# Kernel tuning notes

Measured on AMD Instinct MI355X. Metric: run time of the kernel, lower is better.

Reference implementation:

```python
import jax, jax.numpy as jnp
import numpy as np

NUM_CLASSES = 21
THRESHOLD = 0.5
VAR0, VAR1 = 0.1, 0.2
NEGPOS_RATIO = 3


def setup_inputs() -> dict:
    key = jax.random.key(0)
    k1, k2, k3, k4, k5, k6, k7 = jax.random.split(key, 7)
    B, P, C, O = 64, 8732, 21, 8
    loc_data = jax.random.normal(k1, (B, P, 4), dtype=jnp.float32) * 0.1
    conf_data = jax.random.normal(k2, (B, P, C), dtype=jnp.float32)
    # priors: center form (cx, cy, w, h), valid in [0,1]
    cxy = jax.random.uniform(k3, (P, 2), minval=0.05, maxval=0.95)
    pwh = jax.random.uniform(k4, (P, 2), minval=0.05, maxval=0.3)
    priors = jnp.concatenate([cxy, pwh], axis=-1).astype(jnp.float32)
    # targets: corner-form boxes + class label (float), (B, O, 5)
    tc = jax.random.uniform(k5, (B, O, 2), minval=0.2, maxval=0.8)
    twh = jax.random.uniform(k6, (B, O, 2), minval=0.1, maxval=0.4)
    tmin = jnp.clip(tc - twh / 2, 0.0, 1.0)
    tmax = jnp.clip(tc + twh / 2, 0.0, 1.0)
    labels = jax.random.randint(k7, (B, O, 1), 0, C - 1).astype(jnp.float32)
    targets = jnp.concatenate([tmin, tmax, labels], axis=-1)
    return {"loc_data": loc_data, "conf_data": conf_data, "priors": priors, "targets": targets}


def _point_form(p):
    # (cx,cy,w,h) -> (xmin,ymin,xmax,ymax)
    return jnp.concatenate([p[:, :2] - p[:, 2:] / 2, p[:, :2] + p[:, 2:] / 2], axis=-1)


def _jaccard(a, b):
    # a: (O,4) corners, b: (P,4) corners -> (O,P)
    lt = jnp.maximum(a[:, None, :2], b[None, :, :2])
    rb = jnp.minimum(a[:, None, 2:], b[None, :, 2:])
    wh = jnp.clip(rb - lt, 0.0, None)
    inter = wh[..., 0] * wh[..., 1]
    area_a = ((a[:, 2] - a[:, 0]) * (a[:, 3] - a[:, 1]))[:, None]
    area_b = ((b[:, 2] - b[:, 0]) * (b[:, 3] - b[:, 1]))[None, :]
    return inter / (area_a + area_b - inter)


def _match_one(truths, labels, priors_pt, priors):
    # truths: (O,4) corners, labels: (O,), priors: (P,4) center-form
    ov = _jaccard(truths, priors_pt)                      # (O,P)
    best_prior_idx = jnp.argmax(ov, axis=1)               # (O,)
    best_truth_overlap = jnp.max(ov, axis=0)              # (P,)
    best_truth_idx = jnp.argmax(ov, axis=0)               # (P,)
    # ensure every gt box matches its best prior
    best_truth_overlap = best_truth_overlap.at[best_prior_idx].set(2.0)
    best_truth_idx = best_truth_idx.at[best_prior_idx].set(jnp.arange(truths.shape[0]))
    matched = truths[best_truth_idx]                      # (P,4)
    conf = labels[best_truth_idx].astype(jnp.int32) + 1
    conf = jnp.where(best_truth_overlap < THRESHOLD, 0, conf)
    # encode offsets
    g_cxcy = ((matched[:, :2] + matched[:, 2:]) / 2 - priors[:, :2]) / (VAR0 * priors[:, 2:])
    g_wh = jnp.log(jnp.clip((matched[:, 2:] - matched[:, :2]) / priors[:, 2:], 1e-8, None)) / VAR1
    return jnp.concatenate([g_cxcy, g_wh], axis=-1), conf


def _forward(loc_data, conf_data, priors, targets):
    B, P, C = conf_data.shape
    priors_sg = jax.lax.stop_gradient(priors)             # torch uses .data
    targets_sg = jax.lax.stop_gradient(targets)
    priors_pt = _point_form(priors_sg)
    loc_t, conf_t = jax.vmap(_match_one, in_axes=(0, 0, None, None))(
        targets_sg[:, :, :4], targets_sg[:, :, 4], priors_pt, priors_sg)
    pos = conf_t > 0                                      # (B,P)

    # localization: smooth L1 summed over positive priors
    diff = loc_data - loc_t
    ad = jnp.abs(diff)
    sl1 = jnp.where(ad < 1.0, 0.5 * diff * diff, ad - 0.5)
    loss_l = jnp.sum(sl1 * pos[..., None].astype(sl1.dtype))

    # per-prior conf loss for hard negative mining
    lse = jax.nn.logsumexp(conf_data, axis=-1)            # (B,P)
    gathered = jnp.take_along_axis(conf_data, conf_t[..., None], axis=-1)[..., 0]
    loss_c_all = lse - gathered                           # (B,P)
    mined = jnp.where(pos, 0.0, loss_c_all)
    loss_idx = jnp.argsort(-mined, axis=1)                # descending
    idx_rank = jnp.argsort(loss_idx, axis=1)
    num_pos = jnp.sum(pos.astype(jnp.int32), axis=1, keepdims=True)  # (B,1)
    num_neg = jnp.minimum(NEGPOS_RATIO * num_pos, P - num_pos)
    neg = idx_rank < num_neg                              # (B,P)

    sel = (pos | neg).astype(loss_c_all.dtype)
    loss_c = jnp.sum(loss_c_all * sel)

    N = jnp.sum(num_pos).astype(loss_l.dtype)
    return loss_l / N, loss_c / N


def reference(loc_data, conf_data, priors, targets):
    return _forward(loc_data, conf_data, priors, targets)
```

## Files before the change

### kernel.cpp

```cpp
#include <hip/hip_runtime.h>
#include <math.h>

#define TPB 256
#define TPBS 1024
#define LDSF 12288

typedef unsigned long long ull;
typedef float pf4 __attribute__((ext_vector_type(4), aligned(4)));

__device__ __forceinline__ float jac(float tx0, float ty0, float tx1, float ty1, float ta,
                                     float px0, float py0, float px1, float py1, float pa) {
    float ltx = fmaxf(tx0, px0), lty = fmaxf(ty0, py0);
    float rbx = fminf(tx1, px1), rby = fminf(ty1, py1);
    float w = fmaxf(rbx - ltx, 0.0f), h = fmaxf(rby - lty, 0.0f);
    float inter = w * h;
    return inter / (ta + pa - inter);
}

template <int ON, int CN>
__global__ __launch_bounds__(TPB) void fused_kernel(
    const float* __restrict__ loc, const float* __restrict__ priors,
    const float* __restrict__ targets, const float* __restrict__ conf,
    int P, int O_rt, int C_rt, int CB2,
    float* __restrict__ mined, ull* __restrict__ pkeys,
    float* __restrict__ part_ll, float* __restrict__ part_pc,
    int* __restrict__ part_np) {
    constexpr int OMAX = (ON > 0) ? ON : 64;
    constexpr int CC = (CN > 0) ? CN : 32;
    const int O = (ON > 0) ? ON : O_rt;
    const int C = (CN > 0) ? CN : C_rt;
    const int b = blockIdx.x / CB2;
    const int chunk = blockIdx.x % CB2;
    const int tid = threadIdx.x;
    const int p = chunk * TPB + tid;
    const bool pv = (p < P);
    const int lane = tid & 63, wv = tid >> 6;

    __shared__ float s_tx0[OMAX], s_ty0[OMAX], s_tx1[OMAX], s_ty1[OMAX];
    __shared__ float s_lab[OMAX], s_area[OMAX];
    __shared__ ull s_wk[TPB / 64][OMAX];
    __shared__ float s_wll[TPB / 64], s_wpc[TPB / 64];
    __shared__ int s_wnp[TPB / 64];

    float rv[CC];
    float4 pr4 = make_float4(0.f, 0.f, 1.f, 1.f);
    if (pv) {
        const float* row = conf + ((size_t)b * P + p) * C;
        if (CN > 0) {
#pragma unroll
            for (int q = 0; q < CN / 4; ++q) {
                pf4 v = *(const pf4*)(row + 4 * q);
#pragma unroll
                for (int e = 0; e < 4; ++e) rv[4 * q + e] = v[e];
            }
#pragma unroll
            for (int j = (CN / 4) * 4; j < CN; ++j) rv[j] = row[j];
        } else {
            for (int j = 0; j < C; ++j) rv[j] = row[j];
        }
        pr4 = ((const float4*)priors)[p];
    }

    for (int o = tid; o < O; o += TPB) {
        const float* t = targets + ((size_t)b * O + o) * 5;
        float x0 = t[0], y0 = t[1], x1 = t[2], y1 = t[3];
        s_tx0[o] = x0; s_ty0[o] = y0; s_tx1[o] = x1; s_ty1[o] = y1;
        s_lab[o] = t[4];
        s_area[o] = (x1 - x0) * (y1 - y0);
    }
    __syncthreads();

    float cx = pr4.x, cy = pr4.y, pw = pr4.z, ph = pr4.w;
    float px0 = cx - pw * 0.5f, py0 = cy - ph * 0.5f;
    float px1 = cx + pw * 0.5f, py1 = cy + ph * 0.5f;
    float pa = (px1 - px0) * (py1 - py0);
    float bto = -1.0f;
    int bti = 0;
    for (int o = 0; o < O; ++o) {
        ull kk = 0ull;
        if (pv) {
            float ov = jac(s_tx0[o], s_ty0[o], s_tx1[o], s_ty1[o], s_area[o],
                           px0, py0, px1, py1, pa);
            kk = ((ull)__float_as_uint(ov) << 32) |
                 (ull)(0xFFFFFFFFu - (unsigned)p);
            if (ov > bto) { bto = ov; bti = o; }
        }
#pragma unroll
        for (int d = 1; d < 64; d <<= 1) {
            ull other = __shfl_xor(kk, d, 64);
            if (other > kk) kk = other;
        }
        if (lane == 0) s_wk[wv][o] = kk;
    }
    __syncthreads();
    if (tid < O) {
        ull kk = s_wk[0][tid];
        for (int w = 1; w < TPB / 64; ++w)
            if (s_wk[w][tid] > kk) kk = s_wk[w][tid];
        pkeys[((size_t)b * O + tid) * CB2 + chunk] = kk;
    }

    float ll = 0.0f, pc = 0.0f;
    int np = 0;
    if (pv) {
        float m = rv[0];
#pragma unroll
        for (int j = 1; j < CC; ++j) { if (CN > 0 || j < C) m = fmaxf(m, rv[j]); }
        float s = 0.0f;
#pragma unroll
        for (int j = 0; j < CC; ++j) { if (CN > 0 || j < C) s += expf(rv[j] - m); }
        float lse = m + logf(s);

        int c = (bto < 0.5f) ? 0 : ((int)s_lab[bti] + 1);
        float rowc = rv[0];
#pragma unroll
        for (int j = 1; j < CC; ++j) { if (CN > 0 || j < C) { if (c == j) rowc = rv[j]; } }
        float lc = lse - rowc;

        bool pos = c > 0;
        mined[(size_t)b * P + p] = pos ? 0.0f : lc;
        if (pos) {
            pc = lc;
            np = 1;
            float mx0 = s_tx0[bti], my0 = s_ty0[bti];
            float mx1 = s_tx1[bti], my1 = s_ty1[bti];
            float g0 = ((mx0 + mx1) * 0.5f - cx) / (0.1f * pw);
            float g1 = ((my0 + my1) * 0.5f - cy) / (0.1f * ph);
            float g2 = logf(fmaxf((mx1 - mx0) / pw, 1e-8f)) / 0.2f;
            float g3 = logf(fmaxf((my1 - my0) / ph, 1e-8f)) / 0.2f;
            float4 ld = ((const float4*)loc)[(size_t)b * P + p];
            float gt4[4] = {g0, g1, g2, g3};
            float lv[4] = {ld.x, ld.y, ld.z, ld.w};
#pragma unroll
            for (int q = 0; q < 4; ++q) {
                float d = lv[q] - gt4[q];
                float ad = fabsf(d);
                ll += (ad < 1.0f) ? 0.5f * d * d : (ad - 0.5f);
            }
        }
    }

#pragma unroll
    for (int d = 1; d < 64; d <<= 1) {
        ll += __shfl_xor(ll, d, 64);
        pc += __shfl_xor(pc, d, 64);
        np += __shfl_xor(np, d, 64);
    }
    if (lane == 0) { s_wll[wv] = ll; s_wpc[wv] = pc; s_wnp[wv] = np; }
    __syncthreads();
    if (tid == 0) {
        float L = 0.f, Pc = 0.f;
        int N = 0;
        for (int w = 0; w < TPB / 64; ++w) { L += s_wll[w]; Pc += s_wpc[w]; N += s_wnp[w]; }
        part_ll[blockIdx.x] = L;
        part_pc[blockIdx.x] = Pc;
        part_np[blockIdx.x] = N;
    }
}

template <int ON, int CN>
__global__ __launch_bounds__(TPBS) void select_kernel(
    const float* __restrict__ mined, const float* __restrict__ conf,
    const float* __restrict__ loc, const float* __restrict__ priors,
    const float* __restrict__ targets, const ull* __restrict__ pkeys,
    const float* __restrict__ part_ll, const float* __restrict__ part_pc,
    const int* __restrict__ part_np,
    float* __restrict__ ll_batch, float* __restrict__ lc_batch,
    int* __restrict__ np_batch,
    int P, int O_rt, int C_rt, int CB2, int ratio) {
    constexpr int OMAX = (ON > 0) ? ON : 64;
    const int O = (ON > 0) ? ON : O_rt;
    const int C = (CN > 0) ? CN : C_rt;
    const int b = blockIdx.x, tid = threadIdx.x;
    const int lane = tid & 63, wv = tid >> 6;
    constexpr int W = TPBS / 64;
    const float* v = mined + (size_t)b * P;
    const bool lds = (P <= LDSF);

    __shared__ float s_m[LDSF];
    __shared__ int s_hist[W * 256];
    __shared__ float s_tx0[OMAX], s_ty0[OMAX], s_tx1[OMAX], s_ty1[OMAX];
    __shared__ float s_lab[OMAX], s_area[OMAX];
    __shared__ ull s_keys[OMAX];
    __shared__ int s_bp[OMAX];
    __shared__ float s_wf[W], s_wg[W];
    __shared__ int s_wi[W];
    __shared__ int s_wt[4];
    __shared__ unsigned s_bsel;
    __shared__ int s_krn;
    __shared__ float s_bc[2], s_fix[2];
    __shared__ int s_bn, s_fixn;

    if (lds) {
        for (int i = tid; i < P; i += TPBS) s_m[i] = v[i];
    }
    float pll = 0.0f, ppc = 0.0f;
    int pnp = 0;
    for (int i = tid; i < CB2; i += TPBS) {
        pll += part_ll[b * CB2 + i];
        ppc += part_pc[b * CB2 + i];
        pnp += part_np[b * CB2 + i];
    }
#pragma unroll
    for (int d = 1; d < 64; d <<= 1) {
        pll += __shfl_xor(pll, d, 64);
        ppc += __shfl_xor(ppc, d, 64);
        pnp += __shfl_xor(pnp, d, 64);
    }
    if (lane == 0) { s_wf[wv] = pll; s_wg[wv] = ppc; s_wi[wv] = pnp; }

    if (tid < O) {
        const float* t = targets + ((size_t)b * O + tid) * 5;
        float x0 = t[0], y0 = t[1], x1 = t[2], y1 = t[3];
        s_tx0[tid] = x0; s_ty0[tid] = y0; s_tx1[tid] = x1; s_ty1[tid] = y1;
        s_lab[tid] = t[4];
        s_area[tid] = (x1 - x0) * (y1 - y0);
        s_keys[tid] = 0ull;
    }
    __syncthreads();

    for (int i = tid; i < O * CB2; i += TPBS) {
        int o = i / CB2, s = i % CB2;
        atomicMax(&s_keys[o], pkeys[((size_t)b * O + o) * CB2 + s]);
    }
    __syncthreads();
    if (tid < O)
        s_bp[tid] = (int)(0xFFFFFFFFu - (unsigned)(s_keys[tid] & 0xFFFFFFFFull));
    __syncthreads();

    if (lds && tid < O) s_m[s_bp[tid]] = 0.0f;

    float dll = 0.0f, dpc = 0.0f;
    int dnp = 0;
    if (tid < O) {
        const int o = tid;
        const int p = s_bp[o];
        bool owner = true;
        for (int o2 = o + 1; o2 < O; ++o2)
            if (s_bp[o2] == p) owner = false;
        if (owner) {
            float4 pr = ((const float4*)priors)[p];
            float cx = pr.x, cy = pr.y, pw = pr.z, ph = pr.w;
            float px0 = cx - pw * 0.5f, py0 = cy - ph * 0.5f;
            float px1 = cx + pw * 0.5f, py1 = cy + ph * 0.5f;
            float pa = (px1 - px0) * (py1 - py0);
            float bto = -1.0f;
            int bti = 0;
            for (int o2 = 0; o2 < O; ++o2) {
                float ov = jac(s_tx0[o2], s_ty0[o2], s_tx1[o2], s_ty1[o2], s_area[o2],
                               px0, py0, px1, py1, pa);
                if (ov > bto) { bto = ov; bti = o2; }
            }
            int c_t = (bto < 0.5f) ? 0 : ((int)s_lab[bti] + 1);
            const float* row = conf + ((size_t)b * P + p) * C;
            float m = row[0];
            for (int j = 1; j < C; ++j) m = fmaxf(m, row[j]);
            float s = 0.0f;
            for (int j = 0; j < C; ++j) s += expf(row[j] - m);
            float lse = m + logf(s);
            int c_n = (int)s_lab[o] + 1;
            float lc_n = lse - row[c_n];
            bool pos_t = c_t > 0;
            float lc_t = lse - row[c_t];
            dpc = lc_n - (pos_t ? lc_t : 0.0f);
            dnp = 1 - (pos_t ? 1 : 0);
            float4 ld = ((const float4*)loc)[(size_t)b * P + p];
            float lv[4] = {ld.x, ld.y, ld.z, ld.w};
            float sl_new = 0.0f, sl_old = 0.0f;
            {
                float mx0 = s_tx0[o], my0 = s_ty0[o], mx1 = s_tx1[o], my1 = s_ty1[o];
                float g[4] = {((mx0 + mx1) * 0.5f - cx) / (0.1f * pw),
                              ((my0 + my1) * 0.5f - cy) / (0.1f * ph),
                              logf(fmaxf((mx1 - mx0) / pw, 1e-8f)) / 0.2f,
                              logf(fmaxf((my1 - my0) / ph, 1e-8f)) / 0.2f};
                for (int q = 0; q < 4; ++q) {
                    float d = lv[q] - g[q];
                    float ad = fabsf(d);
                    sl_new += (ad < 1.0f) ? 0.5f * d * d : (ad - 0.5f);
                }
            }
            if (pos_t) {
                float mx0 = s_tx0[bti], my0 = s_ty0[bti], mx1 = s_tx1[bti], my1 = s_ty1[bti];
                float g[4] = {((mx0 + mx1) * 0.5f - cx) / (0.1f * pw),
                              ((my0 + my1) * 0.5f - cy) / (0.1f * ph),
                              logf(fmaxf((mx1 - mx0) / pw, 1e-8f)) / 0.2f,
                              logf(fmaxf((my1 - my0) / ph, 1e-8f)) / 0.2f};
                for (int q = 0; q < 4; ++q) {
                    float d = lv[q] - g[q];
                    float ad = fabsf(d);
                    sl_old += (ad < 1.0f) ? 0.5f * d * d : (ad - 0.5f);
                }
            }
            dll = sl_new - sl_old;
        }
    }
    if (wv == 0) {
#pragma unroll
        for (int d = 1; d < 64; d <<= 1) {
            dll += __shfl_xor(dll, d, 64);
            dpc += __shfl_xor(dpc, d, 64);
            dnp += __shfl_xor(dnp, d, 64);
        }
        if (lane == 0) { s_fix[0] = dll; s_fix[1] = dpc; s_fixn = dnp; }
    }
    __syncthreads();
    if (tid == 0) {
        float L = 0.f, Pc = 0.f;
        int N = 0;
        for (int w = 0; w < W; ++w) { L += s_wf[w]; Pc += s_wg[w]; N += s_wi[w]; }
        s_bc[0] = L + s_fix[0]; s_bc[1] = Pc + s_fix[1]; s_bn = N + s_fixn;
    }
    __syncthreads();
    const float ll_sum = s_bc[0];
    const float sum_pos = s_bc[1];
    const int npos = s_bn;

    const int k = min(ratio * npos, P - npos);
    if (tid == 0) {
        ll_batch[b] = ll_sum;
        np_batch[b] = npos;
    }
    if (k <= 0) {
        if (tid == 0) lc_batch[b] = sum_pos;
        return;
    }

    unsigned prefix = 0u;
    int kr = k;
    for (int pass = 0; pass < 4; ++pass) {
        const int shift = 24 - 8 * pass;
        const unsigned mask = (pass == 0) ? 0u : (0xFFFFFFFFu << (32 - 8 * pass));
        for (int i = tid; i < W * 256; i += TPBS) s_hist[i] = 0;
        __syncthreads();
        for (int i = tid; i < P; i += TPBS) {
            float x;
            if (lds) x = s_m[i];
            else {
                x = v[i];
                for (int o = 0; o < O; ++o)
                    if (i == s_bp[o]) x = 0.0f;
            }
            unsigned u = __float_as_uint(x);
            if ((u & mask) == prefix)
                atomicAdd(&s_hist[wv * 256 + ((u >> shift) & 0xFF)], 1);
        }
        __syncthreads();
        int sge = 0, h = 0;
        if (tid < 256) {
            for (int w = 0; w < W; ++w) h += s_hist[w * 256 + tid];
            int val = h;
#pragma unroll
            for (int d = 1; d < 64; d <<= 1) {
                int t = __shfl_down(val, d, 64);
                if (lane + d < 64) val += t;
            }
            if (lane == 0) s_wt[tid >> 6] = val;
            sge = val;
        }
        __syncthreads();
        if (tid < 256) {
            for (int w = (tid >> 6) + 1; w < 4; ++w) sge += s_wt[w];
            int sgt = sge - h;
            if (sge >= kr && sgt < kr) {
                s_bsel = (unsigned)tid;
                s_krn = kr - sgt;
            }
        }
        __syncthreads();
        prefix |= s_bsel << shift;
        kr = s_krn;
    }
    const float T = __uint_as_float(prefix);
    float lsum = 0.0f;
    int lcnt = 0;
    for (int i = tid; i < P; i += TPBS) {
        float x;
        if (lds) x = s_m[i];
        else {
            x = v[i];
            for (int o = 0; o < O; ++o)
                if (i == s_bp[o]) x = 0.0f;
        }
        if (x > T) { lsum += x; ++lcnt; }
    }
#pragma unroll
    for (int d = 1; d < 64; d <<= 1) {
        lsum += __shfl_xor(lsum, d, 64);
        lcnt += __shfl_xor(lcnt, d, 64);
    }
    if (lane == 0) { s_wf[wv] = lsum; s_wi[wv] = lcnt; }
    __syncthreads();
    if (tid == 0) {
        float S = 0.f;
        int Cn = 0;
        for (int w = 0; w < W; ++w) { S += s_wf[w]; Cn += s_wi[w]; }
        lc_batch[b] = sum_pos + S + (float)(k - Cn) * T;
    }
}

__global__ __launch_bounds__(TPB) void finalize_kernel(
    const float* __restrict__ ll_batch, const int* __restrict__ np_batch,
    const float* __restrict__ lc_batch, int B, float* __restrict__ out) {
    const int tid = threadIdx.x;
    __shared__ float s_l[TPB], s_c[TPB];
    __shared__ int s_n[TPB];
    float l = 0.0f, c = 0.0f;
    int n = 0;
    for (int i = tid; i < B; i += TPB) {
        l += ll_batch[i];
        c += lc_batch[i];
        n += np_batch[i];
    }
    s_l[tid] = l; s_c[tid] = c; s_n[tid] = n;
    __syncthreads();
    for (int s = TPB / 2; s > 0; s >>= 1) {
        if (tid < s) {
            s_l[tid] += s_l[tid + s];
            s_c[tid] += s_c[tid + s];
            s_n[tid] += s_n[tid + s];
        }
        __syncthreads();
    }
    if (tid == 0) {
        float N = (float)s_n[0];
        out[0] = s_l[0] / N;
        out[1] = s_c[0] / N;
    }
}

extern "C" void kernel_launch(void* const* d_in, const int* in_sizes, int n_in,
                              void* d_out, int out_size, void* d_ws, size_t ws_size,
                              hipStream_t stream) {
    const float* loc = (const float*)d_in[0];
    const float* conf = (const float*)d_in[1];
    const float* priors = (const float*)d_in[2];
    const float* targets = (const float*)d_in[3];

    const int P = in_sizes[2] / 4;
    const int B = in_sizes[0] / (P * 4);
    const int C = in_sizes[1] / (in_sizes[0] / 4);
    const int O = in_sizes[3] / (B * 5);
    const size_t BP = (size_t)B * P;
    const int CB2 = (P + TPB - 1) / TPB;

    ull* pkeys = (ull*)d_ws;
    float* mined = (float*)(pkeys + (size_t)B * O * CB2);
    float* part_ll = mined + BP;
    float* part_pc = part_ll + (size_t)B * CB2;
    int* part_np = (int*)(part_pc + (size_t)B * CB2);
    float* ll_batch = (float*)(part_np + (size_t)B * CB2);
    float* lc_batch = ll_batch + B;
    int* np_batch = (int*)(lc_batch + B);

    if (O == 8 && C == 21) {
        fused_kernel<8, 21><<<B * CB2, TPB, 0, stream>>>(
            loc, priors, targets, conf, P, O, C, CB2,
            mined, pkeys, part_ll, part_pc, part_np);
        select_kernel<8, 21><<<B, TPBS, 0, stream>>>(
            mined, conf, loc, priors, targets, pkeys, part_ll, part_pc, part_np,
            ll_batch, lc_batch, np_batch, P, O, C, CB2, 3);
    } else {
        fused_kernel<0, 0><<<B * CB2, TPB, 0, stream>>>(
            loc, priors, targets, conf, P, O, C, CB2,
            mined, pkeys, part_ll, part_pc, part_np);
        select_kernel<0, 0><<<B, TPBS, 0, stream>>>(
            mined, conf, loc, priors, targets, pkeys, part_ll, part_pc, part_np,
            ll_batch, lc_batch, np_batch, P, O, C, CB2, 3);
    }

    finalize_kernel<<<1, TPB, 0, stream>>>(ll_batch, np_batch, lc_batch, B,
                                           (float*)d_out);
}
```

Before: 125.0 us.

## Move best-prior-per-target argmax from fused kernel into select kernel

The fused per-prior kernel no longer does the per-target wavefront shuffle reductions or writes partial best-prior keys to global memory. Instead, each select-kernel block recomputes the IoU of every prior against its batch's targets and reduces the per-target maximum itself, using registers, shuffles and LDS. This removes eight 64-lane shuffle reductions per block, a barrier and the pkeys global round trip from the wide kernel. In exchange, the select kernel, which runs only B blocks, gains an O×P IoU loop and a per-thread key array.

```diff
diff --git a/kernel.cpp b/kernel.cpp
--- a/kernel.cpp
+++ b/kernel.cpp
@@ -22,9 +22,8 @@
     const float* __restrict__ loc, const float* __restrict__ priors,
     const float* __restrict__ targets, const float* __restrict__ conf,
     int P, int O_rt, int C_rt, int CB2,
-    float* __restrict__ mined, ull* __restrict__ pkeys,
-    float* __restrict__ part_ll, float* __restrict__ part_pc,
-    int* __restrict__ part_np) {
+    float* __restrict__ mined, float* __restrict__ part_ll,
+    float* __restrict__ part_pc, int* __restrict__ part_np) {
     constexpr int OMAX = (ON > 0) ? ON : 64;
     constexpr int CC = (CN > 0) ? CN : 32;
     const int O = (ON > 0) ? ON : O_rt;
@@ -38,7 +37,6 @@
 
     __shared__ float s_tx0[OMAX], s_ty0[OMAX], s_tx1[OMAX], s_ty1[OMAX];
     __shared__ float s_lab[OMAX], s_area[OMAX];
-    __shared__ ull s_wk[TPB / 64][OMAX];
     __shared__ float s_wll[TPB / 64], s_wpc[TPB / 64];
     __shared__ int s_wnp[TPB / 64];
 
@@ -70,39 +68,21 @@
     }
     __syncthreads();
 
-    float cx = pr4.x, cy = pr4.y, pw = pr4.z, ph = pr4.w;
-    float px0 = cx - pw * 0.5f, py0 = cy - ph * 0.5f;
-    float px1 = cx + pw * 0.5f, py1 = cy + ph * 0.5f;
-    float pa = (px1 - px0) * (py1 - py0);
-    float bto = -1.0f;
-    int bti = 0;
-    for (int o = 0; o < O; ++o) {
-        ull kk = 0ull;
-        if (pv) {
-            float ov = jac(s_tx0[o], s_ty0[o], s_tx1[o], s_ty1[o], s_area[o],
-                           px0, py0, px1, py1, pa);
-            kk = ((ull)__float_as_uint(ov) << 32) |
-                 (ull)(0xFFFFFFFFu - (unsigned)p);
-            if (ov > bto) { bto = ov; bti = o; }
-        }
-#pragma unroll
-        for (int d = 1; d < 64; d <<= 1) {
-            ull other = __shfl_xor(kk, d, 64);
-            if (other > kk) kk = other;
-        }
-        if (lane == 0) s_wk[wv][o] = kk;
-    }
-    __syncthreads();
-    if (tid < O) {
-        ull kk = s_wk[0][tid];
-        for (int w = 1; w < TPB / 64; ++w)
-            if (s_wk[w][tid] > kk) kk = s_wk[w][tid];
-        pkeys[((size_t)b * O + tid) * CB2 + chunk] = kk;
-    }
-
     float ll = 0.0f, pc = 0.0f;
     int np = 0;
     if (pv) {
+        float cx = pr4.x, cy = pr4.y, pw = pr4.z, ph = pr4.w;
+        float px0 = cx - pw * 0.5f, py0 = cy - ph * 0.5f;
+        float px1 = cx + pw * 0.5f, py1 = cy + ph * 0.5f;
+        float pa = (px1 - px0) * (py1 - py0);
+        float bto = -1.0f;
+        int bti = 0;
+        for (int o = 0; o < O; ++o) {
+            float ov = jac(s_tx0[o], s_ty0[o], s_tx1[o], s_ty1[o], s_area[o],
+                           px0, py0, px1, py1, pa);
+            if (ov > bto) { bto = ov; bti = o; }
+        }
+
         float m = rv[0];
 #pragma unroll
         for (int j = 1; j < CC; ++j) { if (CN > 0 || j < C) m = fmaxf(m, rv[j]); }
@@ -162,7 +142,7 @@
 __global__ __launch_bounds__(TPBS) void select_kernel(
     const float* __restrict__ mined, const float* __restrict__ conf,
     const float* __restrict__ loc, const float* __restrict__ priors,
-    const float* __restrict__ targets, const ull* __restrict__ pkeys,
+    const float* __restrict__ targets,
     const float* __restrict__ part_ll, const float* __restrict__ part_pc,
     const int* __restrict__ part_np,
     float* __restrict__ ll_batch, float* __restrict__ lc_batch,
@@ -179,9 +159,9 @@
 
     __shared__ float s_m[LDSF];
     __shared__ int s_hist[W * 256];
+    __shared__ ull s_wk[W][OMAX];
     __shared__ float s_tx0[OMAX], s_ty0[OMAX], s_tx1[OMAX], s_ty1[OMAX];
     __shared__ float s_lab[OMAX], s_area[OMAX];
-    __shared__ ull s_keys[OMAX];
     __shared__ int s_bp[OMAX];
     __shared__ float s_wf[W], s_wg[W];
     __shared__ int s_wi[W];
@@ -194,6 +174,42 @@
     if (lds) {
         for (int i = tid; i < P; i += TPBS) s_m[i] = v[i];
     }
+    if (tid < O) {
+        const float* t = targets + ((size_t)b * O + tid) * 5;
+        float x0 = t[0], y0 = t[1], x1 = t[2], y1 = t[3];
+        s_tx0[tid] = x0; s_ty0[tid] = y0; s_tx1[tid] = x1; s_ty1[tid] = y1;
+        s_lab[tid] = t[4];
+        s_area[tid] = (x1 - x0) * (y1 - y0);
+    }
+    __syncthreads();
+
+    ull k[OMAX];
+    for (int o = 0; o < O; ++o) k[o] = 0ull;
+    {
+        for (int i = tid; i < P; i += TPBS) {
+            float4 pr = ((const float4*)priors)[i];
+            float px0 = pr.x - pr.z * 0.5f, py0 = pr.y - pr.w * 0.5f;
+            float px1 = pr.x + pr.z * 0.5f, py1 = pr.y + pr.w * 0.5f;
+            float pa = (px1 - px0) * (py1 - py0);
+            for (int o = 0; o < O; ++o) {
+                float ov = jac(s_tx0[o], s_ty0[o], s_tx1[o], s_ty1[o], s_area[o],
+                               px0, py0, px1, py1, pa);
+                ull kk = ((ull)__float_as_uint(ov) << 32) |
+                         (ull)(0xFFFFFFFFu - (unsigned)i);
+                if (kk > k[o]) k[o] = kk;
+            }
+        }
+    }
+    for (int o = 0; o < O; ++o) {
+        ull kk = k[o];
+#pragma unroll
+        for (int d = 32; d > 0; d >>= 1) {
+            ull other = __shfl_down(kk, d, 64);
+            if (other > kk) kk = other;
+        }
+        if (lane == 0) s_wk[wv][o] = kk;
+    }
+
     float pll = 0.0f, ppc = 0.0f;
     int pnp = 0;
     for (int i = tid; i < CB2; i += TPBS) {
@@ -208,24 +224,13 @@
         pnp += __shfl_xor(pnp, d, 64);
     }
     if (lane == 0) { s_wf[wv] = pll; s_wg[wv] = ppc; s_wi[wv] = pnp; }
-
+    __syncthreads();
     if (tid < O) {
-        const float* t = targets + ((size_t)b * O + tid) * 5;
-        float x0 = t[0], y0 = t[1], x1 = t[2], y1 = t[3];
-        s_tx0[tid] = x0; s_ty0[tid] = y0; s_tx1[tid] = x1; s_ty1[tid] = y1;
-        s_lab[tid] = t[4];
-        s_area[tid] = (x1 - x0) * (y1 - y0);
-        s_keys[tid] = 0ull;
-    }
-    __syncthreads();
-
-    for (int i = tid; i < O * CB2; i += TPBS) {
-        int o = i / CB2, s = i % CB2;
-        atomicMax(&s_keys[o], pkeys[((size_t)b * O + o) * CB2 + s]);
-    }
-    __syncthreads();
-    if (tid < O)
-        s_bp[tid] = (int)(0xFFFFFFFFu - (unsigned)(s_keys[tid] & 0xFFFFFFFFull));
+        ull kk = s_wk[0][tid];
+        for (int w = 1; w < W; ++w)
+            if (s_wk[w][tid] > kk) kk = s_wk[w][tid];
+        s_bp[tid] = (int)(0xFFFFFFFFu - (unsigned)(kk & 0xFFFFFFFFull));
+    }
     __syncthreads();
 
     if (lds && tid < O) s_m[s_bp[tid]] = 0.0f;
@@ -315,18 +320,18 @@
     const float sum_pos = s_bc[1];
     const int npos = s_bn;
 
-    const int k = min(ratio * npos, P - npos);
+    const int k2 = min(ratio * npos, P - npos);
     if (tid == 0) {
         ll_batch[b] = ll_sum;
         np_batch[b] = npos;
     }
-    if (k <= 0) {
+    if (k2 <= 0) {
         if (tid == 0) lc_batch[b] = sum_pos;
         return;
     }
 
     unsigned prefix = 0u;
-    int kr = k;
+    int kr = k2;
     for (int pass = 0; pass < 4; ++pass) {
         const int shift = 24 - 8 * pass;
         const unsigned mask = (pass == 0) ? 0u : (0xFFFFFFFFu << (32 - 8 * pass));
@@ -394,7 +399,7 @@
         float S = 0.f;
         int Cn = 0;
         for (int w = 0; w < W; ++w) { S += s_wf[w]; Cn += s_wi[w]; }
-        lc_batch[b] = sum_pos + S + (float)(k - Cn) * T;
+        lc_batch[b] = sum_pos + S + (float)(k2 - Cn) * T;
     }
 }
 
@@ -443,8 +448,7 @@
     const size_t BP = (size_t)B * P;
     const int CB2 = (P + TPB - 1) / TPB;
 
-    ull* pkeys = (ull*)d_ws;
-    float* mined = (float*)(pkeys + (size_t)B * O * CB2);
+    float* mined = (float*)d_ws;
     float* part_ll = mined + BP;
     float* part_pc = part_ll + (size_t)B * CB2;
     int* part_np = (int*)(part_pc + (size_t)B * CB2);
@@ -455,16 +459,16 @@
     if (O == 8 && C == 21) {
         fused_kernel<8, 21><<<B * CB2, TPB, 0, stream>>>(
             loc, priors, targets, conf, P, O, C, CB2,
-            mined, pkeys, part_ll, part_pc, part_np);
+            mined, part_ll, part_pc, part_np);
         select_kernel<8, 21><<<B, TPBS, 0, stream>>>(
-            mined, conf, loc, priors, targets, pkeys, part_ll, part_pc, part_np,
+            mined, conf, loc, priors, targets, part_ll, part_pc, part_np,
             ll_batch, lc_batch, np_batch, P, O, C, CB2, 3);
     } else {
         fused_kernel<0, 0><<<B * CB2, TPB, 0, stream>>>(
             loc, priors, targets, conf, P, O, C, CB2,
-            mined, pkeys, part_ll, part_pc, part_np);
+            mined, part_ll, part_pc, part_np);
         select_kernel<0, 0><<<B, TPBS, 0, stream>>>(
-            mined, conf, loc, priors, targets, pkeys, part_ll, part_pc, part_np,
+            mined, conf, loc, priors, targets, part_ll, part_pc, part_np,
             ll_batch, lc_batch, np_batch, P, O, C, CB2, 3);
     }
 
```

Result: slower. 133.6 us (+6.9%).
